# Performance work log

Measured on AMD Instinct MI355X. Metric: run time of the kernel, lower is better.

## Reference

```python
import jax, jax.numpy as jnp
import numpy as np

B, C, H, W = 2, 4, 32, 256   # batch, num_classes (class 0 = background), range-image H x W
N = H * W                    # candidate points per (batch, class)
RADIUS = 3.0
KM_ITERS = 1
COORD_SCALE = 60.0           # spread lidar x/y so radius-3 NMS is non-trivial


def setup_inputs() -> dict:
    key = jax.random.key(0)
    k1, k2 = jax.random.split(key)
    segmented_channels = jax.random.normal(k1, (B, C, H, W), dtype=jnp.float32)
    lidar = jax.random.normal(k2, (B, 2, H, W), dtype=jnp.float32) * COORD_SCALE
    return {"segmented_channels": segmented_channels, "lidar": lidar}


def _radius_nms(points, mask, radius):
    # Greedy radius NMS in index order: keep point i iff no earlier kept point
    # lies within `radius`. Masked-out points are never kept (keep init = mask).
    n = points.shape[0]
    idx = jnp.arange(n)
    r2 = radius * radius

    def step(keep, i):
        d2 = jnp.sum((points - points[i]) ** 2, axis=-1)       # [N]
        suppress = keep & (d2 < r2) & (idx > i) & keep[i]
        return keep & ~suppress, None

    keep, _ = jax.lax.scan(step, mask, idx)
    return keep


def _kmeans(points, mask, keep, iters):
    # Centers initialized at the NMS-kept points (same index space as points).
    # Each valid class point is assigned to nearest valid center; centers move
    # to the mean of their assigned points.
    n = points.shape[0]
    centers = points
    w = mask.astype(points.dtype)
    BIG = jnp.asarray(1e30, points.dtype)
    for _ in range(iters):
        d2 = jnp.sum((points[:, None, :] - centers[None, :, :]) ** 2, axis=-1)  # [N,N]
        d2 = jnp.where(keep[None, :], d2, BIG)
        assign = jnp.argmin(d2, axis=1)                         # [N]
        sums = jax.ops.segment_sum(points * w[:, None], assign, num_segments=n)
        cnt = jax.ops.segment_sum(w, assign, num_segments=n)
        upd = sums / jnp.maximum(cnt, 1.0)[:, None]
        centers = jnp.where((keep & (cnt > 0))[:, None], upd, centers)
    return centers * keep[:, None].astype(points.dtype)


def reference(segmented_channels, lidar):
    ind = jnp.argmax(segmented_channels, axis=1)                # [B,H,W] class id per cell
    pts = jnp.stack([lidar[:, 0], lidar[:, 1]], axis=-1).reshape(B, N, 2)
    # boolean class masks for foreground classes 1..C-1
    cls_mask = jnp.stack([ind == c for c in range(1, C)], axis=1).reshape(B, C - 1, N)
    pts_all = jnp.broadcast_to(pts[:, None], (B, C - 1, N, 2)).reshape(B * (C - 1), N, 2)
    mask_all = cls_mask.reshape(B * (C - 1), N)

    def per_bc(args):
        p, m = args
        keep = _radius_nms(p, m, RADIUS)
        centers = _kmeans(p, m, keep, KM_ITERS)
        return centers, keep

    centers, keep = jax.lax.map(per_bc, (pts_all, mask_all))
    # centers: padded [B, C-1, N, 2]; keep marks which rows are real detections
    return centers.reshape(B, C - 1, N, 2), keep.reshape(B, C - 1, N)
```

## Files before the change

kernel.cpp:

```cpp
#include <hip/hip_runtime.h>

#define NPTS 8192
#define BCLS 4
#define NP   6
#define R2   9.0f
#define RAD  3.0f
#define GRD  64
#define NCELL (GRD*GRD)
#define PCAP 2048
#define LDSK 2048

#define ST_U 0u
#define ST_A 1u
#define ST_D 2u

__global__ __launch_bounds__(1024) void k_fused(
    const float* __restrict__ seg, const float* __restrict__ lidar,
    float* __restrict__ sumx, float* __restrict__ sumy, float* __restrict__ cntw,
    float* __restrict__ out)
{
    const int p = blockIdx.x;
    const int b = p / 3, cls = p % 3 + 1;
    const int tid = threadIdx.x, lane = tid & 63, wv = tid >> 6;
    const int base = p * NPTS;

    __shared__ float2 sps[NPTS];
    __shared__ unsigned int cmb[NPTS];
    __shared__ unsigned int cellpack[NCELL];
    __shared__ unsigned short plist[2][PCAP];
    __shared__ float ksx[LDSK], ksy[LDSK], kcn[LDSK];
    __shared__ int pcnt[2];
    __shared__ unsigned long long ballots[128];
    __shared__ unsigned int base128[128];
    __shared__ unsigned int wtot[16];
    __shared__ float redbuf[4][16];
    __shared__ float sbminx, sbminy, scell;
    __shared__ int sM, sK;

    float* ok = out + (size_t)2 * NP * NPTS + base;

    for (int k = tid; k < NPTS; k += 1024) { cmb[k] = ST_U; ok[k] = 0.f; }
    {
        float2* oc = (float2*)(out + (size_t)2 * base);
        for (int k = tid; k < NPTS; k += 1024) oc[k] = make_float2(0.f, 0.f);
    }
    for (int k = tid; k < NCELL; k += 1024) cellpack[k] = 0u;
    for (int k = tid; k < LDSK; k += 1024) { ksx[k] = 0.f; ksy[k] = 0.f; kcn[k] = 0.f; }
    if (tid == 0) { pcnt[0] = 0; pcnt[1] = 0; }

    const float* segb = seg + (size_t)b * BCLS * NPTS;
    const float* lx = lidar + (size_t)b * 2 * NPTS;
    const float* ly = lx + NPTS;
    for (int c0 = 0; c0 < 8; ++c0) {
        int n = c0 * 1024 + tid;
        float bv = segb[n];
        int bc = 0;
        #pragma unroll
        for (int c2 = 1; c2 < BCLS; ++c2) {
            float v = segb[c2 * NPTS + n];
            if (v > bv) { bv = v; bc = c2; }
        }
        unsigned long long bal = __ballot(bc == cls);
        if (lane == 0) ballots[c0 * 16 + wv] = bal;
    }
    for (int n = tid; n < NPTS; n += 1024) sps[n] = make_float2(lx[n], ly[n]);
    __syncthreads();
    if (wv == 0) {
        unsigned int s = (unsigned int)__popcll(ballots[2 * lane]) +
                         (unsigned int)__popcll(ballots[2 * lane + 1]);
        for (int d = 1; d < 64; d <<= 1) s += __shfl_xor(s, d, 64);
        if (lane == 0) sM = (int)s;
    }

    const unsigned long long mw = ballots[tid >> 3];
    {
        float mnx = 3e38f, mxx = -3e38f, mny = 3e38f, mxy = -3e38f;
        #pragma unroll
        for (int q = 0; q < 8; ++q) {
            int n = tid * 8 + q;
            bool m = (mw >> (((tid & 7) << 3) + q)) & 1ull;
            float2 c = sps[n];
            if (m) {
                mnx = fminf(mnx, c.x); mxx = fmaxf(mxx, c.x);
                mny = fminf(mny, c.y); mxy = fmaxf(mxy, c.y);
            }
        }
        for (int d = 32; d; d >>= 1) {
            mnx = fminf(mnx, __shfl_xor(mnx, d, 64));
            mxx = fmaxf(mxx, __shfl_xor(mxx, d, 64));
            mny = fminf(mny, __shfl_xor(mny, d, 64));
            mxy = fmaxf(mxy, __shfl_xor(mxy, d, 64));
        }
        if (lane == 0) { redbuf[0][wv] = mnx; redbuf[1][wv] = mxx;
                         redbuf[2][wv] = mny; redbuf[3][wv] = mxy; }
    }
    __syncthreads();
    if (tid == 0) {
        float a = redbuf[0][0], b2 = redbuf[1][0], c = redbuf[2][0], d = redbuf[3][0];
        for (int q = 1; q < 16; ++q) {
            a = fminf(a, redbuf[0][q]); b2 = fmaxf(b2, redbuf[1][q]);
            c = fminf(c, redbuf[2][q]); d = fmaxf(d, redbuf[3][q]);
        }
        sbminx = a; sbminy = c;
        scell = fmaxf(2.0f * RAD, fmaxf(b2 - a, d - c) / 63.0f);
    }
    __syncthreads();
    const float bminx = sbminx, bminy = sbminy, inv = 1.0f / scell;
    const int M = sM;

    float xq[8], yq[8];
    int cellq[8];
    #pragma unroll
    for (int q = 0; q < 8; ++q) {
        int n = tid * 8 + q;
        bool m = (mw >> (((tid & 7) << 3) + q)) & 1ull;
        float2 c = sps[n];
        xq[q] = c.x; yq[q] = c.y;
        int ix = min(GRD - 1, max(0, (int)((c.x - bminx) * inv)));
        int iy = min(GRD - 1, max(0, (int)((c.y - bminy) * inv)));
        cellq[q] = m ? (iy * GRD + ix) : -1;
        if (m) atomicAdd(&cellpack[iy * GRD + ix], 1u);
    }
    __syncthreads();
    {
        unsigned int c4[4], t4 = 0;
        #pragma unroll
        for (int q = 0; q < 4; ++q) { c4[q] = cellpack[tid * 4 + q]; t4 += c4[q]; }
        unsigned int v = t4;
        for (int d = 1; d < 64; d <<= 1) {
            unsigned int u = __shfl_up(v, d, 64);
            if (lane >= d) v += u;
        }
        if (lane == 63) wtot[wv] = v;
        __syncthreads();
        if (tid == 0) {
            unsigned int acc = 0;
            for (int q = 0; q < 16; ++q) { unsigned int t = wtot[q]; wtot[q] = acc; acc += t; }
        }
        __syncthreads();
        unsigned int excl = wtot[wv] + v - t4;
        #pragma unroll
        for (int q = 0; q < 4; ++q) { cellpack[tid * 4 + q] = excl << 16; excl += c4[q]; }
    }
    __syncthreads();
    #pragma unroll
    for (int q = 0; q < 8; ++q) {
        if (cellq[q] >= 0) {
            unsigned int old = atomicAdd(&cellpack[cellq[q]], 1u);
            unsigned int pos = (old >> 16) + (old & 0xffffu);
            sps[pos] = make_float2(xq[q], yq[q]);
            cmb[pos] = ((unsigned int)(tid * 8 + q) << 2) | ST_U;
        }
    }
    __syncthreads();

    #define ROW_FLAGS(CY, CX0, CX1, NI, ME, DEAD, UNDEC)                          \
    {                                                                             \
        unsigned int wa = cellpack[(CY) * GRD + (CX0)];                           \
        unsigned int wb = cellpack[(CY) * GRD + (CX1)];                           \
        unsigned int f0 = wa >> 16, f1 = (wb >> 16) + (wb & 0xffffu);             \
        for (unsigned int f = f0; f < f1; ++f) {                                  \
            unsigned int wf = cmb[f];                                             \
            float2 q = sps[f];                                                    \
            float dx = __fsub_rn((ME).x, q.x), dy = __fsub_rn((ME).y, q.y);       \
            float d2 = __fadd_rn(__fmul_rn(dx, dx), __fmul_rn(dy, dy));           \
            bool in = (d2 < R2) & ((int)(wf >> 2) < (NI));                        \
            DEAD  |= in & ((wf & 3u) == ST_A);                                    \
            UNDEC |= in & ((wf & 3u) == ST_U);                                    \
        }                                                                         \
    }
    #define SCAN_FLAGS(NI, ME, DEAD, UNDEC)                                       \
    {                                                                             \
        int cx0 = max(0, (int)(((ME).x - RAD - bminx) * inv));                    \
        int cx1 = min(GRD - 1, (int)(((ME).x + RAD - bminx) * inv));              \
        int cy0 = max(0, (int)(((ME).y - RAD - bminy) * inv));                    \
        int cy1 = min(GRD - 1, (int)(((ME).y + RAD - bminy) * inv));              \
        DEAD = false; UNDEC = false;                                              \
        ROW_FLAGS(cy0, cx0, cx1, NI, ME, DEAD, UNDEC);                            \
        if (cy1 > cy0) ROW_FLAGS(cy1, cx0, cx1, NI, ME, DEAD, UNDEC);             \
    }

    for (int e = tid; e < M; e += 1024) {
        unsigned int w = cmb[e];
        int ni = (int)(w >> 2);
        float2 me = sps[e];
        bool dead, undec;
        SCAN_FLAGS(ni, me, dead, undec);
        if (dead) cmb[e] = (w & ~3u) | ST_D;
        else if (!undec) cmb[e] = (w & ~3u) | ST_A;
        bool pendf = !dead && undec;
        unsigned long long act = __ballot(true);
        unsigned long long bal = __ballot(pendf);
        int leader = __builtin_ctzll(act);
        int cnt = __popcll(bal);
        int wbase = 0;
        if (lane == leader && cnt) wbase = atomicAdd(&pcnt[0], cnt);
        wbase = __shfl(wbase, leader, 64);
        if (pendf) {
            int pos = wbase + __popcll(bal & ((1ull << lane) - 1ull));
            if (pos < PCAP) plist[0][pos] = (unsigned short)e;
        }
    }

    int cur = 0;
    for (int round = 0; round < NPTS; ++round) {
        __syncthreads();
        int pc = pcnt[cur];
        if (pc == 0) break;
        if (pc > PCAP) {
            for (;;) {
                bool any = false;
                __syncthreads();
                for (int e = tid; e < M; e += 1024) {
                    unsigned int w = cmb[e];
                    if ((w & 3u) != ST_U) continue;
                    int ni = (int)(w >> 2);
                    float2 me = sps[e];
                    bool dead, undec;
                    SCAN_FLAGS(ni, me, dead, undec);
                    if (dead) cmb[e] = (w & ~3u) | ST_D;
                    else if (!undec) cmb[e] = (w & ~3u) | ST_A;
                    else any = true;
                }
                if (__syncthreads_count(any) == 0) break;
            }
            break;
        }
        if (tid == 0) pcnt[cur ^ 1] = 0;
        __syncthreads();
        for (int idx = tid; idx < pc; idx += 1024) {
            int e = plist[cur][idx];
            unsigned int w = cmb[e];
            int ni = (int)(w >> 2);
            float2 me = sps[e];
            bool dead, undec;
            SCAN_FLAGS(ni, me, dead, undec);
            if (dead) cmb[e] = (w & ~3u) | ST_D;
            else if (!undec) cmb[e] = (w & ~3u) | ST_A;
            bool pendf = !dead && undec;
            unsigned long long act = __ballot(true);
            unsigned long long bal = __ballot(pendf);
            int leader = __builtin_ctzll(act);
            int cnt = __popcll(bal);
            int wbase = 0;
            if (lane == leader && cnt) wbase = atomicAdd(&pcnt[cur ^ 1], cnt);
            wbase = __shfl(wbase, leader, 64);
            if (pendf) {
                int pos = wbase + __popcll(bal & ((1ull << lane) - 1ull));
                if (pos < PCAP) plist[cur ^ 1][pos] = (unsigned short)e;
            }
        }
        cur ^= 1;
    }
    __syncthreads();

    for (int k = 0; k < 8; ++k) {
        int e = (k << 10) + tid;
        unsigned long long bal = __ballot((cmb[e] & 3u) == ST_A);
        if (lane == 0) ballots[(k << 4) + wv] = bal;
    }
    __syncthreads();
    if (wv == 0) {
        unsigned int p0 = (unsigned int)__popcll(ballots[2 * lane]);
        unsigned int p1 = (unsigned int)__popcll(ballots[2 * lane + 1]);
        unsigned int s = p0 + p1, v = s;
        for (int d = 1; d < 64; d <<= 1) {
            unsigned int u = __shfl_up(v, d, 64);
            if (lane >= d) v += u;
        }
        base128[2 * lane] = v - s;
        base128[2 * lane + 1] = v - p1;
        if (lane == 63) sK = (int)v;
    }
    __syncthreads();
    #define KRANK(E) ((int)base128[(E) >> 6] +                                    \
                      __popcll(ballots[(E) >> 6] & ((1ull << ((E) & 63)) - 1ull)))
    if (sK > LDSK) {
        for (int k = tid; k < NPTS; k += 1024) {
            sumx[base + k] = 0.f; sumy[base + k] = 0.f; cntw[base + k] = 0.f;
        }
        __syncthreads();
    }

    #define ROW_ARGMIN(CY, CX0, CX1, ME, BD, BE, BN)                              \
    {                                                                             \
        unsigned int wa = cellpack[(CY) * GRD + (CX0)];                           \
        unsigned int wb = cellpack[(CY) * GRD + (CX1)];                           \
        unsigned int f0 = wa >> 16, f1 = (wb >> 16) + (wb & 0xffffu);             \
        for (unsigned int f = f0; f < f1; ++f) {                                  \
            unsigned int wf = cmb[f];                                             \
            float2 q = sps[f];                                                    \
            float dx = __fsub_rn((ME).x, q.x), dy = __fsub_rn((ME).y, q.y);       \
            float d2 = __fadd_rn(__fmul_rn(dx, dx), __fmul_rn(dy, dy));           \
            int nf = (int)(wf >> 2);                                              \
            bool better = ((wf & 3u) == ST_A) &                                   \
                          ((d2 < BD) | ((d2 == BD) & (nf < BN)));                 \
            BD = better ? d2 : BD;                                                \
            BE = better ? (int)f : BE;                                            \
            BN = better ? nf : BN;                                                \
        }                                                                         \
    }
    for (int e = tid; e < M; e += 1024) {
        unsigned int w = cmb[e];
        float2 me = sps[e];
        int be;
        if ((w & 3u) == ST_A) {
            be = e;
        } else {
            int cx0 = max(0, (int)((me.x - RAD - bminx) * inv));
            int cx1 = min(GRD - 1, (int)((me.x + RAD - bminx) * inv));
            int cy0 = max(0, (int)((me.y - RAD - bminy) * inv));
            int cy1 = min(GRD - 1, (int)((me.y + RAD - bminy) * inv));
            float bd = 3e38f;
            be = -1;
            int bn = 1 << 30;
            ROW_ARGMIN(cy0, cx0, cx1, me, bd, be, bn);
            if (cy1 > cy0) ROW_ARGMIN(cy1, cx0, cx1, me, bd, be, bn);
            if (be < 0) continue;
        }
        int r = KRANK(be);
        if (r < LDSK) {
            atomicAdd(&ksx[r], me.x);
            atomicAdd(&ksy[r], me.y);
            atomicAdd(&kcn[r], 1.0f);
        } else {
            atomicAdd(&sumx[base + be], me.x);
            atomicAdd(&sumy[base + be], me.y);
            atomicAdd(&cntw[base + be], 1.0f);
        }
    }
    __syncthreads();

    for (int e = tid; e < M; e += 1024) {
        unsigned int w = cmb[e];
        if ((w & 3u) != ST_A) continue;
        int n = (int)(w >> 2);
        int r = KRANK(e);
        float sx, sy, c;
        if (r < LDSK) { sx = ksx[r]; sy = ksy[r]; c = kcn[r]; }
        else { sx = sumx[base + e]; sy = sumy[base + e]; c = cntw[base + e]; }
        out[2 * (base + n)]     = sx / c;
        out[2 * (base + n) + 1] = sy / c;
        ok[n] = 1.0f;
    }
}

extern "C" void kernel_launch(void* const* d_in, const int* in_sizes, int n_in,
                              void* d_out, int out_size, void* d_ws, size_t ws_size,
                              hipStream_t stream) {
    const float* seg   = (const float*)d_in[0];
    const float* lidar = (const float*)d_in[1];
    float* out = (float*)d_out;

    const size_t A = (size_t)NP * NPTS;
    float* sumx = (float*)d_ws;
    float* sumy = sumx + A;
    float* cntw = sumy + A;

    k_fused<<<NP, 1024, 0, stream>>>(seg, lidar, sumx, sumy, cntw, out);
}
```

Before: 107.0 us.

## Cache undecided-neighbor lists for pending NMS points across rounds

After: 102.1 us. 1.05x faster.

```diff
diff --git a/kernel.cpp b/kernel.cpp
--- a/kernel.cpp
+++ b/kernel.cpp
@@ -9,6 +9,8 @@
 #define NCELL (GRD*GRD)
 #define PCAP 2048
 #define LDSK 2048
+#define NBRPOOL 4096
+#define SCNT 15u
 
 #define ST_U 0u
 #define ST_A 1u
@@ -27,9 +29,10 @@
     __shared__ float2 sps[NPTS];
     __shared__ unsigned int cmb[NPTS];
     __shared__ unsigned int cellpack[NCELL];
-    __shared__ unsigned short plist[2][PCAP];
-    __shared__ float ksx[LDSK], ksy[LDSK], kcn[LDSK];
+    __shared__ unsigned int plist[2][PCAP];
+    __shared__ float kacc[3 * LDSK];
     __shared__ int pcnt[2];
+    __shared__ int nballoc;
     __shared__ unsigned long long ballots[128];
     __shared__ unsigned int base128[128];
     __shared__ unsigned int wtot[16];
@@ -37,6 +40,12 @@
     __shared__ float sbminx, sbminy, scell;
     __shared__ int sM, sK;
 
+    unsigned short* scratch = (unsigned short*)kacc;
+    unsigned short* nbr = ((unsigned short*)kacc) + 8192;
+    float* ksx = kacc;
+    float* ksy = kacc + LDSK;
+    float* kcn = kacc + 2 * LDSK;
+
     float* ok = out + (size_t)2 * NP * NPTS + base;
 
     for (int k = tid; k < NPTS; k += 1024) { cmb[k] = ST_U; ok[k] = 0.f; }
@@ -45,8 +54,7 @@
         for (int k = tid; k < NPTS; k += 1024) oc[k] = make_float2(0.f, 0.f);
     }
     for (int k = tid; k < NCELL; k += 1024) cellpack[k] = 0u;
-    for (int k = tid; k < LDSK; k += 1024) { ksx[k] = 0.f; ksy[k] = 0.f; kcn[k] = 0.f; }
-    if (tid == 0) { pcnt[0] = 0; pcnt[1] = 0; }
+    if (tid == 0) { pcnt[0] = 0; pcnt[1] = 0; nballoc = 0; }
 
     const float* segb = seg + (size_t)b * BCLS * NPTS;
     const float* lx = lidar + (size_t)b * 2 * NPTS;
@@ -178,6 +186,25 @@
         DEAD = false; UNDEC = false;                                              \
         ROW_FLAGS(cy0, cx0, cx1, NI, ME, DEAD, UNDEC);                            \
         if (cy1 > cy0) ROW_FLAGS(cy1, cx0, cx1, NI, ME, DEAD, UNDEC);             \
+    }
+
+    #define ROW_COLLECT(CY, CX0, CX1, NI, ME, DEAD, UCNT, SBASE)                  \
+    {                                                                             \
+        unsigned int wa = cellpack[(CY) * GRD + (CX0)];                           \
+        unsigned int wb = cellpack[(CY) * GRD + (CX1)];                           \
+        unsigned int f0 = wa >> 16, f1 = (wb >> 16) + (wb & 0xffffu);             \
+        for (unsigned int f = f0; f < f1; ++f) {                                  \
+            unsigned int wf = cmb[f];                                             \
+            float2 q = sps[f];                                                    \
+            float dx = __fsub_rn((ME).x, q.x), dy = __fsub_rn((ME).y, q.y);       \
+            float d2 = __fadd_rn(__fmul_rn(dx, dx), __fmul_rn(dy, dy));           \
+            bool in = (d2 < R2) & ((int)(wf >> 2) < (NI));                        \
+            DEAD |= in & ((wf & 3u) == ST_A);                                     \
+            if (in & ((wf & 3u) == ST_U)) {                                       \
+                if (UCNT < 8u) scratch[(SBASE) + UCNT] = (unsigned short)f;       \
+                ++UCNT;                                                           \
+            }                                                                     \
+        }                                                                         \
     }
 
     for (int e = tid; e < M; e += 1024) {
@@ -198,7 +225,7 @@
         wbase = __shfl(wbase, leader, 64);
         if (pendf) {
             int pos = wbase + __popcll(bal & ((1ull << lane) - 1ull));
-            if (pos < PCAP) plist[0][pos] = (unsigned short)e;
+            if (pos < PCAP) plist[0][pos] = (unsigned int)e | (SCNT << 13);
         }
     }
 
@@ -229,15 +256,52 @@
         if (tid == 0) pcnt[cur ^ 1] = 0;
         __syncthreads();
         for (int idx = tid; idx < pc; idx += 1024) {
-            int e = plist[cur][idx];
+            unsigned int rec = plist[cur][idx];
+            int e = (int)(rec & 0x1FFFu);
+            unsigned int lcnt = (rec >> 13) & 15u;
+            unsigned int off = rec >> 17;
             unsigned int w = cmb[e];
-            int ni = (int)(w >> 2);
-            float2 me = sps[e];
-            bool dead, undec;
-            SCAN_FLAGS(ni, me, dead, undec);
-            if (dead) cmb[e] = (w & ~3u) | ST_D;
-            else if (!undec) cmb[e] = (w & ~3u) | ST_A;
-            bool pendf = !dead && undec;
+            bool pendf = false;
+            unsigned int newrec = 0;
+            if (lcnt == SCNT) {
+                int ni = (int)(w >> 2);
+                float2 me = sps[e];
+                int cx0 = max(0, (int)((me.x - RAD - bminx) * inv));
+                int cx1 = min(GRD - 1, (int)((me.x + RAD - bminx) * inv));
+                int cy0 = max(0, (int)((me.y - RAD - bminy) * inv));
+                int cy1 = min(GRD - 1, (int)((me.y + RAD - bminy) * inv));
+                bool dead = false;
+                unsigned int ucnt = 0;
+                const int sbase = tid * 8;
+                ROW_COLLECT(cy0, cx0, cx1, ni, me, dead, ucnt, sbase);
+                if (cy1 > cy0) ROW_COLLECT(cy1, cx0, cx1, ni, me, dead, ucnt, sbase);
+                if (dead) cmb[e] = (w & ~3u) | ST_D;
+                else if (ucnt == 0) cmb[e] = (w & ~3u) | ST_A;
+                else {
+                    pendf = true;
+                    newrec = (unsigned int)e | (SCNT << 13);
+                    if (ucnt <= 8u) {
+                        int o = atomicAdd(&nballoc, (int)ucnt);
+                        if (o + (int)ucnt <= NBRPOOL) {
+                            for (unsigned int c = 0; c < ucnt; ++c)
+                                nbr[o + c] = scratch[sbase + c];
+                            newrec = (unsigned int)e | (ucnt << 13) | ((unsigned int)o << 17);
+                        }
+                    }
+                }
+            } else {
+                bool dead = false;
+                unsigned int k2 = 0;
+                for (unsigned int c = 0; c < lcnt; ++c) {
+                    unsigned short f = nbr[off + c];
+                    unsigned int st = cmb[f] & 3u;
+                    if (st == ST_A) { dead = true; break; }
+                    if (st == ST_U) nbr[off + k2++] = f;
+                }
+                if (dead) cmb[e] = (w & ~3u) | ST_D;
+                else if (k2 == 0) cmb[e] = (w & ~3u) | ST_A;
+                else { pendf = true; newrec = (unsigned int)e | (k2 << 13) | (off << 17); }
+            }
             unsigned long long act = __ballot(true);
             unsigned long long bal = __ballot(pendf);
             int leader = __builtin_ctzll(act);
@@ -247,13 +311,14 @@
             wbase = __shfl(wbase, leader, 64);
             if (pendf) {
                 int pos = wbase + __popcll(bal & ((1ull << lane) - 1ull));
-                if (pos < PCAP) plist[cur ^ 1][pos] = (unsigned short)e;
+                if (pos < PCAP) plist[cur ^ 1][pos] = newrec;
             }
         }
         cur ^= 1;
     }
     __syncthreads();
 
+    for (int k = tid; k < 3 * LDSK; k += 1024) kacc[k] = 0.f;
     for (int k = 0; k < 8; ++k) {
         int e = (k << 10) + tid;
         unsigned long long bal = __ballot((cmb[e] & 3u) == ST_A);
```

## Split argmax/compaction into a wide front kernel feeding per-class NMS kernel

Applied to the files above, without the earlier changes.

Measured after the change: 105.9 us. Within noise of the previous version (-1.1%).

```diff
diff --git a/kernel.cpp b/kernel.cpp
--- a/kernel.cpp
+++ b/kernel.cpp
@@ -9,18 +9,93 @@
 #define NCELL (GRD*GRD)
 #define PCAP 2048
 #define LDSK 2048
+#define KBLK 64
+#define KTHR 256
 
 #define ST_U 0u
 #define ST_A 1u
 #define ST_D 2u
 
-__global__ __launch_bounds__(1024) void k_fused(
+
+__global__ __launch_bounds__(KTHR) void k_front(
     const float* __restrict__ seg, const float* __restrict__ lidar,
-    float* __restrict__ sumx, float* __restrict__ sumy, float* __restrict__ cntw,
+    float* __restrict__ xs, float* __restrict__ ys,
+    unsigned int* __restrict__ ns, unsigned int* __restrict__ counts,
+    float* __restrict__ out)
+{
+    const int tid = threadIdx.x, lane = tid & 63;
+    const int idx = blockIdx.x * KTHR + tid;
+    const int b = idx >> 13, n = idx & 8191;
+
+    __shared__ float ex[KTHR], ey[KTHR];
+    __shared__ unsigned short en[KTHR];
+    __shared__ unsigned int cnt6[6], off6[6], pos6[6];
+
+    if (tid < 6) cnt6[tid] = 0;
+    __syncthreads();
+
+    const float* segb = seg + (size_t)b * BCLS * NPTS + n;
+    float bv = segb[0];
+    int bc = 0;
+    #pragma unroll
+    for (int c = 1; c < BCLS; ++c) {
+        float v = segb[(size_t)c * NPTS];
+        if (v > bv) { bv = v; bc = c; }
+    }
+    const float x = lidar[(size_t)b * 2 * NPTS + n];
+    const float y = lidar[(size_t)b * 2 * NPTS + NPTS + n];
+    const int p = (bc > 0) ? (b * 3 + bc - 1) : -1;
+
+    #pragma unroll
+    for (int q = 0; q < 6; ++q) {
+        unsigned long long bal = __ballot(p == q);
+        if (lane == 0 && bal) atomicAdd(&cnt6[q], (unsigned int)__popcll(bal));
+    }
+    __syncthreads();
+    if (tid == 0) {
+        unsigned int a = 0;
+        #pragma unroll
+        for (int q = 0; q < 6; ++q) { off6[q] = a; pos6[q] = a; a += cnt6[q]; }
+    }
+    __syncthreads();
+    #pragma unroll
+    for (int q = 0; q < 6; ++q) {
+        unsigned long long bal = __ballot(p == q);
+        if (bal) {
+            int ldr = __builtin_ctzll(bal);
+            unsigned int wb = 0;
+            if (lane == ldr) wb = atomicAdd(&pos6[q], (unsigned int)__popcll(bal));
+            wb = __shfl(wb, ldr, 64);
+            if (p == q) {
+                unsigned int s = wb + (unsigned int)__popcll(bal & ((1ull << lane) - 1ull));
+                ex[s] = x; ey[s] = y; en[s] = (unsigned short)n;
+            }
+        }
+    }
+    __syncthreads();
+    {
+        const unsigned int total = off6[5] + cnt6[5];
+        const int gbase = blockIdx.x * KTHR;
+        for (int k = tid; k < (int)total; k += KTHR) {
+            xs[gbase + k] = ex[k];
+            ys[gbase + k] = ey[k];
+            ns[gbase + k] = (unsigned int)en[k];
+        }
+        if (tid < 6) counts[blockIdx.x * 6 + tid] = cnt6[tid];
+    }
+    {
+        float4* o4 = (float4*)out;
+        for (int k = idx; k < 36864; k += KBLK * KTHR)
+            o4[k] = make_float4(0.f, 0.f, 0.f, 0.f);
+    }
+}
+
+__global__ __launch_bounds__(1024) void k_nms(
+    const float* __restrict__ xs, const float* __restrict__ ys,
+    const unsigned int* __restrict__ ns, const unsigned int* __restrict__ counts,
     float* __restrict__ out)
 {
     const int p = blockIdx.x;
-    const int b = p / 3, cls = p % 3 + 1;
     const int tid = threadIdx.x, lane = tid & 63, wv = tid >> 6;
     const int base = p * NPTS;
 
@@ -34,55 +109,58 @@
     __shared__ unsigned int base128[128];
     __shared__ unsigned int wtot[16];
     __shared__ float redbuf[4][16];
+    __shared__ unsigned int csrc[KBLK], cdst[KBLK], clen[KBLK];
     __shared__ float sbminx, sbminy, scell;
     __shared__ int sM, sK;
 
     float* ok = out + (size_t)2 * NP * NPTS + base;
 
-    for (int k = tid; k < NPTS; k += 1024) { cmb[k] = ST_U; ok[k] = 0.f; }
-    {
-        float2* oc = (float2*)(out + (size_t)2 * base);
-        for (int k = tid; k < NPTS; k += 1024) oc[k] = make_float2(0.f, 0.f);
-    }
+    for (int k = tid; k < NPTS; k += 1024) cmb[k] = ST_U;
     for (int k = tid; k < NCELL; k += 1024) cellpack[k] = 0u;
     for (int k = tid; k < LDSK; k += 1024) { ksx[k] = 0.f; ksy[k] = 0.f; kcn[k] = 0.f; }
     if (tid == 0) { pcnt[0] = 0; pcnt[1] = 0; }
 
-    const float* segb = seg + (size_t)b * BCLS * NPTS;
-    const float* lx = lidar + (size_t)b * 2 * NPTS;
-    const float* ly = lx + NPTS;
-    for (int c0 = 0; c0 < 8; ++c0) {
-        int n = c0 * 1024 + tid;
-        float bv = segb[n];
-        int bc = 0;
+    if (wv == 0) {
+        unsigned int c6[6];
         #pragma unroll
-        for (int c2 = 1; c2 < BCLS; ++c2) {
-            float v = segb[c2 * NPTS + n];
-            if (v > bv) { bv = v; bc = c2; }
-        }
-        unsigned long long bal = __ballot(bc == cls);
-        if (lane == 0) ballots[c0 * 16 + wv] = bal;
-    }
-    for (int n = tid; n < NPTS; n += 1024) sps[n] = make_float2(lx[n], ly[n]);
-    __syncthreads();
-    if (wv == 0) {
-        unsigned int s = (unsigned int)__popcll(ballots[2 * lane]) +
-                         (unsigned int)__popcll(ballots[2 * lane + 1]);
-        for (int d = 1; d < 64; d <<= 1) s += __shfl_xor(s, d, 64);
-        if (lane == 0) sM = (int)s;
-    }
-
-    const unsigned long long mw = ballots[tid >> 3];
+        for (int q = 0; q < 6; ++q) c6[q] = counts[lane * 6 + q];
+        unsigned int within = 0;
+        for (int q = 0; q < p; ++q) within += c6[q];
+        unsigned int len = c6[p];
+        unsigned int v = len;
+        for (int d = 1; d < 64; d <<= 1) {
+            unsigned int u = __shfl_up(v, d, 64);
+            if (lane >= d) v += u;
+        }
+        csrc[lane] = lane * KTHR + within;
+        cdst[lane] = v - len;
+        clen[lane] = len;
+        if (lane == 63) sM = (int)v;
+    }
+    __syncthreads();
+    const int M = sM;
+
+    float xq[8], yq[8];
+    unsigned int nq[8];
+    int liq[8];
     {
         float mnx = 3e38f, mxx = -3e38f, mny = 3e38f, mxy = -3e38f;
         #pragma unroll
         for (int q = 0; q < 8; ++q) {
-            int n = tid * 8 + q;
-            bool m = (mw >> (((tid & 7) << 3) + q)) & 1ull;
-            float2 c = sps[n];
-            if (m) {
-                mnx = fminf(mnx, c.x); mxx = fmaxf(mxx, c.x);
-                mny = fminf(mny, c.y); mxy = fmaxf(mxy, c.y);
+            int li = q * 1024 + tid;
+            liq[q] = li;
+            if (li < M) {
+                int lo = 0, hi = KBLK - 1;
+                #pragma unroll
+                for (int s = 0; s < 6; ++s) {
+                    int mid = (lo + hi + 1) >> 1;
+                    if (cdst[mid] <= (unsigned int)li) lo = mid; else hi = mid - 1;
+                }
+                int si = csrc[lo] + (li - cdst[lo]);
+                float x = xs[si], y = ys[si];
+                xq[q] = x; yq[q] = y; nq[q] = ns[si];
+                mnx = fminf(mnx, x); mxx = fmaxf(mxx, x);
+                mny = fminf(mny, y); mxy = fmaxf(mxy, y);
             }
         }
         for (int d = 32; d; d >>= 1) {
@@ -106,20 +184,16 @@
     }
     __syncthreads();
     const float bminx = sbminx, bminy = sbminy, inv = 1.0f / scell;
-    const int M = sM;
-
-    float xq[8], yq[8];
+
     int cellq[8];
     #pragma unroll
     for (int q = 0; q < 8; ++q) {
-        int n = tid * 8 + q;
-        bool m = (mw >> (((tid & 7) << 3) + q)) & 1ull;
-        float2 c = sps[n];
-        xq[q] = c.x; yq[q] = c.y;
-        int ix = min(GRD - 1, max(0, (int)((c.x - bminx) * inv)));
-        int iy = min(GRD - 1, max(0, (int)((c.y - bminy) * inv)));
-        cellq[q] = m ? (iy * GRD + ix) : -1;
-        if (m) atomicAdd(&cellpack[iy * GRD + ix], 1u);
+        if (liq[q] < M) {
+            int ix = min(GRD - 1, max(0, (int)((xq[q] - bminx) * inv)));
+            int iy = min(GRD - 1, max(0, (int)((yq[q] - bminy) * inv)));
+            cellq[q] = iy * GRD + ix;
+            atomicAdd(&cellpack[cellq[q]], 1u);
+        } else cellq[q] = -1;
     }
     __syncthreads();
     {
@@ -149,7 +223,7 @@
             unsigned int old = atomicAdd(&cellpack[cellq[q]], 1u);
             unsigned int pos = (old >> 16) + (old & 0xffffu);
             sps[pos] = make_float2(xq[q], yq[q]);
-            cmb[pos] = ((unsigned int)(tid * 8 + q) << 2) | ST_U;
+            cmb[pos] = (nq[q] << 2) | ST_U;
         }
     }
     __syncthreads();
@@ -275,12 +349,6 @@
     __syncthreads();
     #define KRANK(E) ((int)base128[(E) >> 6] +                                    \
                       __popcll(ballots[(E) >> 6] & ((1ull << ((E) & 63)) - 1ull)))
-    if (sK > LDSK) {
-        for (int k = tid; k < NPTS; k += 1024) {
-            sumx[base + k] = 0.f; sumy[base + k] = 0.f; cntw[base + k] = 0.f;
-        }
-        __syncthreads();
-    }
 
     #define ROW_ARGMIN(CY, CX0, CX1, ME, BD, BE, BN)                              \
     {                                                                             \
@@ -300,48 +368,51 @@
             BN = better ? nf : BN;                                                \
         }                                                                         \
     }
-    for (int e = tid; e < M; e += 1024) {
-        unsigned int w = cmb[e];
-        float2 me = sps[e];
-        int be;
-        if ((w & 3u) == ST_A) {
-            be = e;
-        } else {
-            int cx0 = max(0, (int)((me.x - RAD - bminx) * inv));
-            int cx1 = min(GRD - 1, (int)((me.x + RAD - bminx) * inv));
-            int cy0 = max(0, (int)((me.y - RAD - bminy) * inv));
-            int cy1 = min(GRD - 1, (int)((me.y + RAD - bminy) * inv));
-            float bd = 3e38f;
-            be = -1;
-            int bn = 1 << 30;
-            ROW_ARGMIN(cy0, cx0, cx1, me, bd, be, bn);
-            if (cy1 > cy0) ROW_ARGMIN(cy1, cx0, cx1, me, bd, be, bn);
-            if (be < 0) continue;
-        }
-        int r = KRANK(be);
-        if (r < LDSK) {
-            atomicAdd(&ksx[r], me.x);
-            atomicAdd(&ksy[r], me.y);
-            atomicAdd(&kcn[r], 1.0f);
-        } else {
-            atomicAdd(&sumx[base + be], me.x);
-            atomicAdd(&sumy[base + be], me.y);
-            atomicAdd(&cntw[base + be], 1.0f);
-        }
-    }
-    __syncthreads();
-
-    for (int e = tid; e < M; e += 1024) {
-        unsigned int w = cmb[e];
-        if ((w & 3u) != ST_A) continue;
-        int n = (int)(w >> 2);
-        int r = KRANK(e);
-        float sx, sy, c;
-        if (r < LDSK) { sx = ksx[r]; sy = ksy[r]; c = kcn[r]; }
-        else { sx = sumx[base + e]; sy = sumy[base + e]; c = cntw[base + e]; }
-        out[2 * (base + n)]     = sx / c;
-        out[2 * (base + n) + 1] = sy / c;
-        ok[n] = 1.0f;
+    const int npass = (sK + LDSK - 1) / LDSK;
+    for (int pass = 0; pass < npass; ++pass) {
+        const int rb = pass * LDSK;
+        if (pass) {
+            __syncthreads();
+            for (int k = tid; k < LDSK; k += 1024) { ksx[k] = 0.f; ksy[k] = 0.f; kcn[k] = 0.f; }
+        }
+        __syncthreads();
+        for (int e = tid; e < M; e += 1024) {
+            unsigned int w = cmb[e];
+            float2 me = sps[e];
+            int be;
+            if ((w & 3u) == ST_A) {
+                be = e;
+            } else {
+                int cx0 = max(0, (int)((me.x - RAD - bminx) * inv));
+                int cx1 = min(GRD - 1, (int)((me.x + RAD - bminx) * inv));
+                int cy0 = max(0, (int)((me.y - RAD - bminy) * inv));
+                int cy1 = min(GRD - 1, (int)((me.y + RAD - bminy) * inv));
+                float bd = 3e38f;
+                be = -1;
+                int bn = 1 << 30;
+                ROW_ARGMIN(cy0, cx0, cx1, me, bd, be, bn);
+                if (cy1 > cy0) ROW_ARGMIN(cy1, cx0, cx1, me, bd, be, bn);
+                if (be < 0) continue;
+            }
+            int r = KRANK(be) - rb;
+            if (r >= 0 && r < LDSK) {
+                atomicAdd(&ksx[r], me.x);
+                atomicAdd(&ksy[r], me.y);
+                atomicAdd(&kcn[r], 1.0f);
+            }
+        }
+        __syncthreads();
+        for (int e = tid; e < M; e += 1024) {
+            unsigned int w = cmb[e];
+            if ((w & 3u) != ST_A) continue;
+            int r = KRANK(e) - rb;
+            if (r < 0 || r >= LDSK) continue;
+            int n = (int)(w >> 2);
+            float sx = ksx[r], sy = ksy[r], c = kcn[r];
+            out[2 * (base + n)]     = sx / c;
+            out[2 * (base + n) + 1] = sy / c;
+            ok[n] = 1.0f;
+        }
     }
 }
 
@@ -352,10 +423,11 @@
     const float* lidar = (const float*)d_in[1];
     float* out = (float*)d_out;
 
-    const size_t A = (size_t)NP * NPTS;
-    float* sumx = (float*)d_ws;
-    float* sumy = sumx + A;
-    float* cntw = sumy + A;
-
-    k_fused<<<NP, 1024, 0, stream>>>(seg, lidar, sumx, sumy, cntw, out);
+    float* xs = (float*)d_ws;
+    float* ys = xs + KBLK * KTHR;
+    unsigned int* ns = (unsigned int*)(ys + KBLK * KTHR);
+    unsigned int* counts = ns + KBLK * KTHR;
+
+    k_front<<<KBLK, KTHR, 0, stream>>>(seg, lidar, xs, ys, ns, counts, out);
+    k_nms<<<NP, 1024, 0, stream>>>(xs, ys, ns, counts, out);
 }
```
